# Performance work log

Hardware: AMD Instinct MI355X
Metric: run time of the kernel (lower is better)

Reference implementation:

```python
import jax, jax.numpy as jnp
import numpy as np

H, KD, VD, KNN = 8, 64, 64, 128
D, FC, N, S = 512, 2048, 4, 1024
GW_DEC, GW_ENC = 0.5, 0.5
EPS = 1e-5
SCALE = float(np.sqrt(KD))


def _layer_norm(x):
    # nn.LayerNorm(out_dim, eps=1e-5, elementwise_affine=False)
    m = jnp.mean(x, -1, keepdims=True)
    v = jnp.var(x, -1, keepdims=True)
    return (x - m) * jax.lax.rsqrt(v + EPS)


def _mha(x, Wk, bk, Wv, bv, Wo, bo, att_graph, gw, mask, Wq=None, bq=None, q_in=None):
    # x: [N,S,D]; per-head projections stacked: Wk [H,D,Kd], Wv [H,D,Vd]
    key = jnp.einsum('nsd,hdk->hnsk', x, Wk) + bk[:, None, None, :]
    value = jnp.einsum('nsd,hdv->hnsv', x, Wv) + bv[:, None, None, :]
    if q_in is None:
        query = key  # self-attention: query = key (as in the torch code)
    else:
        query = jnp.einsum('nqd,hdk->hnqk', q_in, Wq) + bq[:, None, None, :]
    # broadcast-mul-sum in torch == batched matmul
    att = jnp.einsum('hnqk,hnsk->hnqs', query, key) / SCALE  # [H,N,Q,S]
    if mask:
        qlen, slen = att.shape[-2], att.shape[-1]
        causal = jnp.arange(slen)[None, :] <= jnp.arange(qlen)[:, None]
        att = jnp.where(causal, att, -jnp.inf)
    # knn sparsification: keep top-KNN per row, rest -> -inf (equiv to topk+scatter for distinct values)
    thresh = jax.lax.top_k(att, KNN)[0][..., -1:]
    att = jnp.where(att >= thresh, att, -jnp.inf)
    att = jax.nn.softmax(att, axis=-1)
    # blend with precomputed (softmaxed) graph attention
    att = gw * att_graph + (1.0 - gw) * att
    ctx = jnp.einsum('hnqs,hnsv->hnqv', att, value)  # [H,N,Q,Vd]
    ctx = jnp.transpose(ctx, (1, 2, 0, 3)).reshape(ctx.shape[1], ctx.shape[2], H * VD)
    return ctx @ Wo + bo


def setup_inputs() -> dict:
    key = jax.random.key(0)
    ks = jax.random.split(key, 22)
    p = lambda k, shp: (0.02 * jax.random.normal(k, shp)).astype(jnp.float32)
    return {
        'z': jax.random.normal(ks[0], (N, S, D), jnp.float32),
        'y': jax.random.normal(ks[1], (N, S, D), jnp.float32),
        'graph_dec': jax.random.normal(ks[2], (S, S), jnp.float32),
        'graph_enc': jax.random.normal(ks[3], (S, S), jnp.float32),
        'dec_Wk': p(ks[4], (H, D, KD)), 'dec_bk': p(ks[5], (H, KD)),
        'dec_Wv': p(ks[6], (H, D, VD)), 'dec_bv': p(ks[7], (H, VD)),
        'dec_Wo': p(ks[8], (H * VD, D)), 'dec_bo': p(ks[9], (D,)),
        'enc_Wk': p(ks[10], (H, D, KD)), 'enc_bk': p(ks[11], (H, KD)),
        'enc_Wq': p(ks[12], (H, D, KD)), 'enc_bq': p(ks[13], (H, KD)),
        'enc_Wv': p(ks[14], (H, D, VD)), 'enc_bv': p(ks[15], (H, VD)),
        'enc_Wo': p(ks[16], (H * VD, D)), 'enc_bo': p(ks[17], (D,)),
        'fc_W1': p(ks[18], (D, FC)), 'fc_b1': p(ks[19], (FC,)),
        'fc_W2': p(ks[20], (FC, D)), 'fc_b2': p(ks[21], (D,)),
    }


def reference(z, y, graph_dec, graph_enc, dec_Wk, dec_bk, dec_Wv, dec_bv, dec_Wo, dec_bo, enc_Wk, enc_bk, enc_Wq, enc_bq, enc_Wv, enc_bv, enc_Wo, enc_bo, fc_W1, fc_b1, fc_W2, fc_b2):
    # graphs are row-softmaxed at construction time in the torch module
    gdec = jax.nn.softmax(graph_dec, axis=-1)
    genc = jax.nn.softmax(graph_enc, axis=-1)
    # 1) masked decoder self-attention on y
    h = _mha(y, dec_Wk, dec_bk, dec_Wv, dec_bv, dec_Wo, dec_bo, gdec, GW_DEC, True)
    h = _layer_norm(h + y)
    # 2) encoder-decoder attention: keys/values from z, query from h via query_keys (query_key=True)
    h2 = _mha(z, enc_Wk, enc_bk, enc_Wv, enc_bv, enc_Wo, enc_bo, genc, GW_ENC, False, enc_Wq, enc_bq, h)
    h2 = _layer_norm(h2 + h)
    # 3) two-layer MLP
    h3 = jax.nn.relu(h2 @ fc_W1 + fc_b1) @ fc_W2 + fc_b2
    return _layer_norm(h3 + h2)
```

## Files before the change

kernel.cpp:

```cpp
#include <hip/hip_runtime.h>
#include <stdint.h>

typedef short short8 __attribute__((ext_vector_type(8)));
typedef short short4v __attribute__((ext_vector_type(4)));
typedef float floatx4 __attribute__((ext_vector_type(4)));

#define H_  8
#define NB_ 4
#define S_  1024
#define D_  512
#define KD_ 64

__device__ __forceinline__ short f2bf(float f){
    unsigned u = __builtin_bit_cast(unsigned, f);
    u += 0x7fffu + ((u>>16)&1u);
    return (short)(u>>16);
}
__device__ __forceinline__ float wred_addf(float x){
    #pragma unroll
    for(int o=32;o>0;o>>=1) x += __shfl_xor(x,o,64);
    return x;
}
__device__ __forceinline__ float wred_maxf(float x){
    #pragma unroll
    for(int o=32;o>0;o>>=1) x = fmaxf(x,__shfl_xor(x,o,64));
    return x;
}
__device__ __forceinline__ unsigned bkey(unsigned u){
    return (u & 0x8000u) ? ((~u) & 0xffffu) : (u | 0x8000u);
}
__device__ __forceinline__ float key2f(unsigned k){
    unsigned u = (k & 0x8000u) ? (k & 0x7fffu) : ((~k) & 0xffffu);
    return __builtin_bit_cast(float, u<<16);
}

__global__ __launch_bounds__(256) void cvt2_kernel(const float* __restrict__ a, const float* __restrict__ b,
                                                   short* __restrict__ oa, short* __restrict__ ob){
    const float* in = blockIdx.y ? b : a;
    short* out = blockIdx.y ? ob : oa;
    int i = (blockIdx.x*256 + threadIdx.x)*4;
    floatx4 v = *(const floatx4*)(in + i);
    short4v r;
    #pragma unroll
    for(int j=0;j<4;j++) r[j] = f2bf(v[j]);
    *(short4v*)(out + i) = r;
}

__global__ __launch_bounds__(256) void wtrans5_kernel(
    const float* __restrict__ dWk, const float* __restrict__ dWv,
    const float* __restrict__ eWk, const float* __restrict__ eWv, const float* __restrict__ eWq,
    short* __restrict__ wKVd, short* __restrict__ wKVe, short* __restrict__ wQet)
{
    __shared__ float t[32][33];
    int zz = blockIdx.z; int w = zz>>3, h = zz&7;
    const float* src; short* dst;
    if(w==0){ src = dWk + h*32768; dst = wKVd + h*65536; }
    else if(w==1){ src = dWv + h*32768; dst = wKVd + h*65536 + 32768; }
    else if(w==2){ src = eWk + h*32768; dst = wKVe + h*65536; }
    else if(w==3){ src = eWv + h*32768; dst = wKVe + h*65536 + 32768; }
    else { src = eWq + h*32768; dst = wQet + h*32768; }
    const int R = 512, C = 64;
    int c0 = blockIdx.x*32, r0 = blockIdx.y*32;
    int tid = threadIdx.x;
    int r = tid>>3, cq = (tid&7)*4;
    #pragma unroll
    for(int i=0;i<4;i++) t[r][cq+i] = src[(r0+r)*C + c0+cq+i];
    __syncthreads();
    int c = tid>>3, rq = (tid&7)*4;
    #pragma unroll
    for(int i=0;i<4;i++) dst[(c0+c)*R + r0+rq+i] = f2bf(t[rq+i][c]);
}

__global__ __launch_bounds__(256) void wtrans4_kernel(
    const float* __restrict__ dWo, const float* __restrict__ eWo,
    const float* __restrict__ W1, const float* __restrict__ W2,
    short* __restrict__ oWod, short* __restrict__ oWoe,
    short* __restrict__ oW1, short* __restrict__ oW2)
{
    __shared__ float t[32][33];
    int id = blockIdx.x;
    const float* src; short* dst; int R, C, c0, r0;
    if(id < 512){
        src = (id<256)? dWo : eWo; dst = (id<256)? oWod : oWoe;
        int tt = id & 255; R = 512; C = 512;
        c0 = (tt&15)*32; r0 = (tt>>4)*32;
    } else if(id < 1536){
        src = W1; dst = oW1; int tt = id - 512; R = 512; C = 2048;
        c0 = (tt&63)*32; r0 = (tt>>6)*32;
    } else {
        src = W2; dst = oW2; int tt = id - 1536; R = 2048; C = 512;
        c0 = (tt&15)*32; r0 = (tt>>4)*32;
    }
    int tid = threadIdx.x;
    int r = tid>>3, cq = (tid&7)*4;
    #pragma unroll
    for(int i=0;i<4;i++) t[r][cq+i] = src[(long)(r0+r)*C + c0+cq+i];
    __syncthreads();
    int c = tid>>3, rq = (tid&7)*4;
    #pragma unroll
    for(int i=0;i<4;i++) dst[(long)(c0+c)*R + r0+rq+i] = f2bf(t[rq+i][c]);
}

__global__ __launch_bounds__(256) void graph_softmax_kernel(const float* __restrict__ g0,
                                                            const float* __restrict__ g1,
                                                            short* __restrict__ o0,
                                                            short* __restrict__ o1){
    int row = blockIdx.x;
    const float* g = blockIdx.y ? g1 : g0;
    short* o = blockIdx.y ? o1 : o0;
    const float* gr = g + (long)row*S_;
    short* orow = o + (long)row*S_;
    int tid = threadIdx.x, wave = tid>>6, lane = tid&63;
    __shared__ float red[8];
    float v[4]; float mx = -3.0e38f;
    #pragma unroll
    for(int i=0;i<4;i++){ v[i] = gr[tid + 256*i]; mx = fmaxf(mx, v[i]); }
    mx = wred_maxf(mx);
    if(lane==0) red[wave] = mx;
    __syncthreads();
    mx = fmaxf(fmaxf(red[0],red[1]), fmaxf(red[2],red[3]));
    float s = 0.f;
    #pragma unroll
    for(int i=0;i<4;i++){ v[i] = __expf(v[i]-mx); s += v[i]; }
    s = wred_addf(s);
    if(lane==0) red[4+wave] = s;
    __syncthreads();
    s = red[4]+red[5]+red[6]+red[7];
    float inv = 1.f/s;
    #pragma unroll
    for(int i=0;i<4;i++) orow[tid + 256*i] = f2bf(v[i]*inv);
}

template<int KV>
__global__ __launch_bounds__(256) void gemm_proj_kernel(
    const short* __restrict__ A, const short* __restrict__ Bt,
    const float* __restrict__ b1, const float* __restrict__ b2,
    short* __restrict__ o1, short* __restrict__ o2)
{
    constexpr int TN = KV ? 128 : 64;
    constexpr int NI = TN/32;
    __shared__ short As[64*32];
    __shared__ short Bs[TN*32];
    int z = blockIdx.z;
    int m0 = blockIdx.x*64;
    const short* Bb = Bt + (long)z*(TN*512);
    int tid = threadIdx.x, wave = tid>>6, lane = tid&63, quad = lane>>4, nl = lane&15;
    int wm = (wave&1)*32, wn = (wave>>1)*(TN/2);
    floatx4 acc[2][NI];
    #pragma unroll
    for(int i=0;i<2;i++)
        #pragma unroll
        for(int j=0;j<NI;j++) acc[i][j] = (floatx4){0.f,0.f,0.f,0.f};
    int r = tid>>2, c = (tid&3)*8;
    for(int k0=0;k0<512;k0+=32){
        __syncthreads();
        __builtin_amdgcn_global_load_lds(
            (const __attribute__((address_space(1))) unsigned*)(A + (long)(m0 + r)*512 + k0 + c),
            (__attribute__((address_space(3))) unsigned*)((char*)As + wave*1024), 16, 0, 0);
        #pragma unroll
        for(int i=0;i<TN/64;i++)
            __builtin_amdgcn_global_load_lds(
                (const __attribute__((address_space(1))) unsigned*)(Bb + (long)(r + i*64)*512 + k0 + c),
                (__attribute__((address_space(3))) unsigned*)((char*)Bs + i*4096 + wave*1024), 16, 0, 0);
        __syncthreads();
        short8 af[2], bfr[NI];
        #pragma unroll
        for(int i=0;i<2;i++) af[i] = *(const short8*)(As + (wm + i*16 + nl)*32 + quad*8);
        #pragma unroll
        for(int j=0;j<NI;j++) bfr[j] = *(const short8*)(Bs + (wn + j*16 + nl)*32 + quad*8);
        #pragma unroll
        for(int i=0;i<2;i++)
            #pragma unroll
            for(int j=0;j<NI;j++)
                acc[i][j] = __builtin_amdgcn_mfma_f32_16x16x32_bf16(af[i],bfr[j],acc[i][j],0,0,0);
    }
    #pragma unroll
    for(int j=0;j<NI;j++){
        int n = wn + j*16 + nl;
        float bv = (KV && n >= 64) ? b2[z*64 + n - 64] : b1[z*64 + n];
        #pragma unroll
        for(int i=0;i<2;i++){
            #pragma unroll
            for(int rr=0;rr<4;rr++){
                int m = m0 + wm + i*16 + quad*4 + rr;
                float v = acc[i][j][rr] + bv;
                long zb = (long)(z*NB_ + (m>>10));
                if(KV && n >= 64) o2[ (zb*KD_ + (n-64))*S_ + (m&1023) ] = f2bf(v);
                else              o1[ (zb*S_ + (m&1023))*KD_ + n ] = f2bf(v);
            }
        }
    }
}

template<int TM, int TN, int OUTBF, int RELU>
__global__ __launch_bounds__(256) void gemm_big_kernel(
    const short* __restrict__ A, const short* __restrict__ Bt, const float* __restrict__ bias,
    void* __restrict__ out, int M, int N, int K)
{
    __shared__ short As[TM*32];
    __shared__ short Bs[TN*32];
    int m0 = blockIdx.x*TM, n0 = blockIdx.y*TN;
    int tid = threadIdx.x, wave = tid>>6, lane = tid&63, quad = lane>>4, nl = lane&15;
    constexpr int MI = TM/32, NI = TN/32;
    int wm = (wave&1)*(TM/2), wn = (wave>>1)*(TN/2);
    floatx4 acc[MI][NI];
    #pragma unroll
    for(int i=0;i<MI;i++)
        #pragma unroll
        for(int j=0;j<NI;j++) acc[i][j] = (floatx4){0.f,0.f,0.f,0.f};

    int r = tid>>2, c = (tid&3)*8;
    for(int k0=0;k0<K;k0+=32){
        __syncthreads();
        #pragma unroll
        for(int i=0;i<TM/64;i++)
            __builtin_amdgcn_global_load_lds(
                (const __attribute__((address_space(1))) unsigned*)(A + (long)(m0 + r + i*64)*K + k0 + c),
                (__attribute__((address_space(3))) unsigned*)((char*)As + i*4096 + wave*1024),
                16, 0, 0);
        #pragma unroll
        for(int i=0;i<TN/64;i++)
            __builtin_amdgcn_global_load_lds(
                (const __attribute__((address_space(1))) unsigned*)(Bt + (long)(n0 + r + i*64)*K + k0 + c),
                (__attribute__((address_space(3))) unsigned*)((char*)Bs + i*4096 + wave*1024),
                16, 0, 0);
        __syncthreads();
        short8 af[MI], bfr[NI];
        #pragma unroll
        for(int i=0;i<MI;i++) af[i] = *(const short8*)(As + (wm + i*16 + nl)*32 + quad*8);
        #pragma unroll
        for(int j=0;j<NI;j++) bfr[j] = *(const short8*)(Bs + (wn + j*16 + nl)*32 + quad*8);
        #pragma unroll
        for(int i=0;i<MI;i++)
            #pragma unroll
            for(int j=0;j<NI;j++)
                acc[i][j] = __builtin_amdgcn_mfma_f32_16x16x32_bf16(af[i],bfr[j],acc[i][j],0,0,0);
    }
    #pragma unroll
    for(int j=0;j<NI;j++){
        int n = n0 + wn + j*16 + nl;
        float bv = bias[n];
        #pragma unroll
        for(int i=0;i<MI;i++){
            #pragma unroll
            for(int rr=0;rr<4;rr++){
                int m = m0 + wm + i*16 + quad*4 + rr;
                float v = acc[i][j][rr] + bv;
                if(RELU) v = fmaxf(v, 0.f);
                if(OUTBF) ((short*)out)[(long)m*N + n] = f2bf(v);
                else      ((float*)out)[(long)m*N + n] = v;
            }
        }
    }
}

__global__ __launch_bounds__(512,6) void attn_kernel(
    const short* __restrict__ Qb, const short* __restrict__ Kb, const short* __restrict__ Vt,
    const short* __restrict__ graph, short* __restrict__ ctx, int causal)
{
    __shared__ short attb[16*1024];
    __shared__ float pbuf[16*68];
    int hn = blockIdx.x, qt = blockIdx.y;
    int h = hn>>2, n = hn&3;
    int q0 = qt*16;
    int tid=threadIdx.x, wave=tid>>6, lane=tid&63, quad=lane>>4, nl=lane&15;

    const short* Qp = Qb + ((long)hn*S_ + q0 + nl)*KD_ + quad*8;
    short8 aq0 = *(const short8*)(Qp);
    short8 aq1 = *(const short8*)(Qp + 32);
    const short* Kp = Kb + (long)hn*S_*KD_;
    int stmax = causal ? qt : 63;
    for(int st=wave; st<=stmax; st+=8){
        const short* kp = Kp + (st*16 + nl)*KD_ + quad*8;
        short8 b0 = *(const short8*)(kp);
        short8 b1 = *(const short8*)(kp + 32);
        floatx4 cc = (floatx4){0.f,0.f,0.f,0.f};
        cc = __builtin_amdgcn_mfma_f32_16x16x32_bf16(aq0,b0,cc,0,0,0);
        cc = __builtin_amdgcn_mfma_f32_16x16x32_bf16(aq1,b1,cc,0,0,0);
        #pragma unroll
        for(int rr=0;rr<4;rr++){
            int q = quad*4 + rr, s = st*16 + nl;
            attb[q*1024 + ((s + 8*q)&1023)] = f2bf(cc[rr]*0.125f);
        }
    }
    __syncthreads();

    for(int rp=0; rp<2; ++rp){
        int q = wave*2 + rp;
        int qg = q0 + q;
        int slimit = causal ? qg : 1023;
        short* rowp = attb + q*1024;
        int sb = lane*16;
        int p0 = (sb + 8*q) & 1023;
        short8 c0 = *(const short8*)(rowp + p0);
        short8 c1 = *(const short8*)(rowp + ((p0+8)&1023));
        unsigned mv[16];
        unsigned mk = 0u;
        #pragma unroll
        for(int j=0;j<8;j++){
            unsigned k0 = (sb+j   <= slimit) ? bkey((unsigned)(unsigned short)c0[j]) : 0u;
            unsigned k1 = (sb+8+j <= slimit) ? bkey((unsigned)(unsigned short)c1[j]) : 0u;
            mv[j]   = k0; mk = k0>mk?k0:mk;
            mv[8+j] = k1; mk = k1>mk?k1:mk;
        }
        #pragma unroll
        for(int o=32;o>0;o>>=1){ unsigned tt=__shfl_xor(mk,o,64); mk = tt>mk?tt:mk; }
        unsigned lo=0u, hi=mk+1u;
        for(int it=0; it<16; ++it){
            unsigned mid = lo + ((hi-lo)>>1);
            unsigned cnt = 0u;
            #pragma unroll
            for(int j=0;j<16;j++) cnt += (mv[j] >= mid) ? 1u : 0u;
            #pragma unroll
            for(int o=32;o>0;o>>=1) cnt += __shfl_xor(cnt,o,64);
            bool ge = (cnt >= 128u);
            bool eq = (cnt == 128u);
            lo = ge ? mid : lo;
            hi = ge ? (eq ? mid+1u : hi) : mid;
        }
        float mxf = key2f(mk);
        float sm = 0.f;
        #pragma unroll
        for(int j=0;j<16;j++){
            unsigned k = mv[j];
            float e = (k >= lo && k != 0u) ? __expf(key2f(k)-mxf) : 0.f;
            mv[j] = __builtin_bit_cast(unsigned, e);
            sm += e;
        }
        #pragma unroll
        for(int o=32;o>0;o>>=1) sm += __shfl_xor(sm,o,64);
        float inv = 0.5f/sm;
        const short* grow = graph + (long)qg*1024 + sb;
        short8 g0 = *(const short8*)(grow);
        short8 g1 = *(const short8*)(grow + 8);
        short8 o0, o1;
        #pragma unroll
        for(int j=0;j<8;j++){
            float gv0 = __builtin_bit_cast(float, ((unsigned)(unsigned short)g0[j])<<16);
            float gv1 = __builtin_bit_cast(float, ((unsigned)(unsigned short)g1[j])<<16);
            float e0 = __builtin_bit_cast(float, mv[j]);
            float e1 = __builtin_bit_cast(float, mv[8+j]);
            o0[j] = f2bf(0.5f*gv0 + e0*inv);
            o1[j] = f2bf(0.5f*gv1 + e1*inv);
        }
        *(short8*)(rowp + p0) = o0;
        *(short8*)(rowp + ((p0+8)&1023)) = o1;
    }
    __syncthreads();

    int vh = wave & 3, sh = wave >> 2;
    int v0 = vh*16;
    const short* Vp = Vt + ((long)hn*KD_ + v0 + nl)*S_;
    floatx4 o4 = (floatx4){0.f,0.f,0.f,0.f};
    int arow = nl;
    int sbase = sh*512;
    for(int s0=sbase; s0<sbase+512; s0+=32){
        int cs = (s0 + quad*8 + 8*arow) & 1023;
        short8 ap = *(const short8*)(attb + arow*1024 + cs);
        short8 bv = *(const short8*)(Vp + s0 + quad*8);
        o4 = __builtin_amdgcn_mfma_f32_16x16x32_bf16(ap,bv,o4,0,0,0);
    }
    if(sh==1){
        #pragma unroll
        for(int rr=0;rr<4;rr++) pbuf[(quad*4+rr)*68 + v0 + nl] = o4[rr];
    }
    __syncthreads();
    if(sh==0){
        #pragma unroll
        for(int rr=0;rr<4;rr++){
            int q = quad*4 + rr;
            float v = o4[rr] + pbuf[q*68 + v0 + nl];
            ctx[ ((long)(n*S_ + q0 + q))*512 + h*KD_ + v0 + nl ] = f2bf(v);
        }
    }
}

__global__ __launch_bounds__(256) void ln_kernel(const float* __restrict__ x, const float* __restrict__ res,
                                                 float* __restrict__ outf, short* __restrict__ outb){
    long row = blockIdx.x;
    const float* xr = x + row*D_;
    const float* rr = res + row*D_;
    int tid = threadIdx.x, wave = tid>>6, lane = tid&63;
    float t0 = xr[tid] + rr[tid];
    float t1 = xr[tid+256] + rr[tid+256];
    float s = t0 + t1, s2 = t0*t0 + t1*t1;
    __shared__ float red[8];
    s = wred_addf(s); s2 = wred_addf(s2);
    if(lane==0){ red[wave] = s; red[4+wave] = s2; }
    __syncthreads();
    s  = red[0]+red[1]+red[2]+red[3];
    s2 = red[4]+red[5]+red[6]+red[7];
    float mean = s*(1.f/512.f);
    float var = s2*(1.f/512.f) - mean*mean;
    float rs = rsqrtf(var + 1e-5f);
    float o0 = (t0-mean)*rs, o1 = (t1-mean)*rs;
    if(outf){ outf[row*D_+tid] = o0; outf[row*D_+tid+256] = o1; }
    if(outb){ outb[row*D_+tid] = f2bf(o0); outb[row*D_+tid+256] = f2bf(o1); }
}

extern "C" void kernel_launch(void* const* d_in, const int* in_sizes, int n_in,
                              void* d_out, int out_size, void* d_ws, size_t ws_size,
                              hipStream_t stream)
{
    const float* z         = (const float*)d_in[0];
    const float* y         = (const float*)d_in[1];
    const float* graph_dec = (const float*)d_in[2];
    const float* graph_enc = (const float*)d_in[3];
    const float* dec_Wk = (const float*)d_in[4];  const float* dec_bk = (const float*)d_in[5];
    const float* dec_Wv = (const float*)d_in[6];  const float* dec_bv = (const float*)d_in[7];
    const float* dec_Wo = (const float*)d_in[8];  const float* dec_bo = (const float*)d_in[9];
    const float* enc_Wk = (const float*)d_in[10]; const float* enc_bk = (const float*)d_in[11];
    const float* enc_Wq = (const float*)d_in[12]; const float* enc_bq = (const float*)d_in[13];
    const float* enc_Wv = (const float*)d_in[14]; const float* enc_bv = (const float*)d_in[15];
    const float* enc_Wo = (const float*)d_in[16]; const float* enc_bo = (const float*)d_in[17];
    const float* fc_W1  = (const float*)d_in[18]; const float* fc_b1  = (const float*)d_in[19];
    const float* fc_W2  = (const float*)d_in[20]; const float* fc_b2  = (const float*)d_in[21];

    char* ws = (char*)d_ws;
    short* gdec  = (short*)(ws + 0x0000000);
    short* genc  = (short*)(ws + 0x0400000);
    short* y_bf  = (short*)(ws + 0x0800000);
    short* z_bf  = (short*)(ws + 0x0C00000);
    short* Kdec  = (short*)(ws + 0x1000000);
    short* Vtdec = (short*)(ws + 0x1400000);
    short* Kenc  = (short*)(ws + 0x1800000);
    short* Vtenc = (short*)(ws + 0x1C00000);
    short* Qenc  = (short*)(ws + 0x2000000);
    short* ctx   = (short*)(ws + 0x2400000);
    float* tmp   = (float*)(ws + 0x2800000);
    float* hbuf  = (float*)(ws + 0x3000000);
    short* h_bf  = (short*)(ws + 0x3800000);
    float* h2    = (float*)(ws + 0x3C00000);
    short* h2_bf = (short*)(ws + 0x4400000);
    short* fc1   = (short*)(ws + 0x4800000);
    short* wKVd  = (short*)(ws + 0x5800000);
    short* wKVe  = (short*)(ws + 0x5900000);
    short* wQet  = (short*)(ws + 0x5A00000);
    short* wOdt  = (short*)(ws + 0x5A80000);
    short* wOet  = (short*)(ws + 0x5B00000);
    short* wF1t  = (short*)(ws + 0x5B80000);
    short* wF2t  = (short*)(ws + 0x5D80000);
    float* outp  = (float*)d_out;

    dim3 B(256);
    wtrans5_kernel<<<dim3(2,16,40),B,0,stream>>>(dec_Wk, dec_Wv, enc_Wk, enc_Wv, enc_Wq, wKVd, wKVe, wQet);
    wtrans4_kernel<<<dim3(2560),B,0,stream>>>(dec_Wo, enc_Wo, fc_W1, fc_W2, wOdt, wOet, wF1t, wF2t);
    cvt2_kernel<<<dim3(2048,2),B,0,stream>>>(y, z, y_bf, z_bf);
    graph_softmax_kernel<<<dim3(1024,2),B,0,stream>>>(graph_dec, graph_enc, gdec, genc);
    gemm_proj_kernel<1><<<dim3(64,1,8),B,0,stream>>>(y_bf, wKVd, dec_bk, dec_bv, Kdec, Vtdec);
    attn_kernel<<<dim3(32,64),dim3(512),0,stream>>>(Kdec, Kdec, Vtdec, gdec, ctx, 1);
    gemm_big_kernel<64,128,0,0><<<dim3(64,4),B,0,stream>>>(ctx, wOdt, dec_bo, tmp, 4096, 512, 512);
    ln_kernel<<<dim3(4096),B,0,stream>>>(tmp, y, hbuf, h_bf);
    gemm_proj_kernel<1><<<dim3(64,1,8),B,0,stream>>>(z_bf, wKVe, enc_bk, enc_bv, Kenc, Vtenc);
    gemm_proj_kernel<0><<<dim3(64,1,8),B,0,stream>>>(h_bf, wQet, enc_bq, (const float*)0, Qenc, (short*)0);
    attn_kernel<<<dim3(32,64),dim3(512),0,stream>>>(Qenc, Kenc, Vtenc, genc, ctx, 0);
    gemm_big_kernel<64,128,0,0><<<dim3(64,4),B,0,stream>>>(ctx, wOet, enc_bo, tmp, 4096, 512, 512);
    ln_kernel<<<dim3(4096),B,0,stream>>>(tmp, hbuf, h2, h2_bf);
    gemm_big_kernel<128,128,1,1><<<dim3(32,16),B,0,stream>>>(h2_bf, wF1t, fc_b1, fc1, 4096, 2048, 512);
    gemm_big_kernel<64,128,0,0><<<dim3(64,4),B,0,stream>>>(fc1, wF2t, fc_b2, tmp, 4096, 512, 2048);
    ln_kernel<<<dim3(4096),B,0,stream>>>(tmp, h2, outp, (short*)0);
}
```

Before: 429.4 us.

## Speed up attention top-k selection with DPP reductions and packed bf16 math

Rewrites the per-row top-k threshold and softmax blend in the attention kernel. It uses DPP-based wave reductions instead of shuffles, packed bit tricks for the bf16 key transform, and a binary search that exits early once the range narrows. Causal masking is now applied by pre-filling and writing -inf in the score buffer, so the per-element masking branch in the selection loop goes away. The 0.5 graph weight is folded into the graph softmax, and packed bf16 conversion is used on output. There are risks: the pre-fill adds an extra barrier and LDS store pass for causal blocks, and the search loop now has a data-dependent trip count.

```diff
diff --git a/kernel.cpp b/kernel.cpp
--- a/kernel.cpp
+++ b/kernel.cpp
@@ -4,6 +4,7 @@
 typedef short short8 __attribute__((ext_vector_type(8)));
 typedef short short4v __attribute__((ext_vector_type(4)));
 typedef float floatx4 __attribute__((ext_vector_type(4)));
+typedef unsigned uint4v __attribute__((ext_vector_type(4)));
 
 #define H_  8
 #define NB_ 4
@@ -26,12 +27,46 @@
     for(int o=32;o>0;o>>=1) x = fmaxf(x,__shfl_xor(x,o,64));
     return x;
 }
-__device__ __forceinline__ unsigned bkey(unsigned u){
-    return (u & 0x8000u) ? ((~u) & 0xffffu) : (u | 0x8000u);
-}
-__device__ __forceinline__ float key2f(unsigned k){
-    unsigned u = (k & 0x8000u) ? (k & 0x7fffu) : ((~k) & 0xffffu);
-    return __builtin_bit_cast(float, u<<16);
+__device__ __forceinline__ unsigned umaxu(unsigned a, unsigned b){ return a>b?a:b; }
+
+template<int CTRL, int RMASK, int BC>
+__device__ __forceinline__ unsigned dppu(unsigned x){
+    return (unsigned)__builtin_amdgcn_update_dpp(0, (int)x, CTRL, RMASK, 0xf, BC);
+}
+__device__ __forceinline__ unsigned wsum_dpp_u(unsigned x){
+    x += dppu<0x111,0xf,1>(x);
+    x += dppu<0x112,0xf,1>(x);
+    x += dppu<0x114,0xf,1>(x);
+    x += dppu<0x118,0xf,1>(x);
+    x += dppu<0x142,0xa,0>(x);
+    x += dppu<0x143,0xc,0>(x);
+    return (unsigned)__builtin_amdgcn_readlane((int)x, 63);
+}
+__device__ __forceinline__ unsigned wmax_dpp_u(unsigned x){
+    x = umaxu(x, dppu<0x111,0xf,1>(x));
+    x = umaxu(x, dppu<0x112,0xf,1>(x));
+    x = umaxu(x, dppu<0x114,0xf,1>(x));
+    x = umaxu(x, dppu<0x118,0xf,1>(x));
+    x = umaxu(x, dppu<0x142,0xa,0>(x));
+    x = umaxu(x, dppu<0x143,0xc,0>(x));
+    return (unsigned)__builtin_amdgcn_readlane((int)x, 63);
+}
+__device__ __forceinline__ float addu_f(float a, unsigned b){
+    return a + __builtin_bit_cast(float, b);
+}
+__device__ __forceinline__ float wsum_dpp_f(float x){
+    x = addu_f(x, dppu<0x111,0xf,1>(__builtin_bit_cast(unsigned,x)));
+    x = addu_f(x, dppu<0x112,0xf,1>(__builtin_bit_cast(unsigned,x)));
+    x = addu_f(x, dppu<0x114,0xf,1>(__builtin_bit_cast(unsigned,x)));
+    x = addu_f(x, dppu<0x118,0xf,1>(__builtin_bit_cast(unsigned,x)));
+    x = addu_f(x, dppu<0x142,0xa,0>(__builtin_bit_cast(unsigned,x)));
+    x = addu_f(x, dppu<0x143,0xc,0>(__builtin_bit_cast(unsigned,x)));
+    return __builtin_bit_cast(float, (unsigned)__builtin_amdgcn_readlane((int)__builtin_bit_cast(unsigned, x), 63));
+}
+__device__ __forceinline__ unsigned cvt_pk_bf16(float a, float b){
+    unsigned r;
+    asm("v_cvt_pk_bf16_f32 %0, %1, %2" : "=v"(r) : "v"(a), "v"(b));
+    return r;
 }
 
 __global__ __launch_bounds__(256) void cvt2_kernel(const float* __restrict__ a, const float* __restrict__ b,
@@ -126,7 +161,7 @@
     if(lane==0) red[4+wave] = s;
     __syncthreads();
     s = red[4]+red[5]+red[6]+red[7];
-    float inv = 1.f/s;
+    float inv = 0.5f/s;
     #pragma unroll
     for(int i=0;i<4;i++) orow[tid + 256*i] = f2bf(v[i]*inv);
 }
@@ -265,6 +300,13 @@
     int q0 = qt*16;
     int tid=threadIdx.x, wave=tid>>6, lane=tid&63, quad=lane>>4, nl=lane&15;
 
+    if(causal){
+        uint4v fv = (uint4v){0xff80ff80u,0xff80ff80u,0xff80ff80u,0xff80ff80u};
+        #pragma unroll
+        for(int i=0;i<4;i++) *(uint4v*)((char*)attb + tid*16 + i*8192) = fv;
+        __syncthreads();
+    }
+
     const short* Qp = Qb + ((long)hn*S_ + q0 + nl)*KD_ + quad*8;
     short8 aq0 = *(const short8*)(Qp);
     short8 aq1 = *(const short8*)(Qp + 32);
@@ -277,74 +319,86 @@
         floatx4 cc = (floatx4){0.f,0.f,0.f,0.f};
         cc = __builtin_amdgcn_mfma_f32_16x16x32_bf16(aq0,b0,cc,0,0,0);
         cc = __builtin_amdgcn_mfma_f32_16x16x32_bf16(aq1,b1,cc,0,0,0);
+        int s = st*16 + nl;
         #pragma unroll
         for(int rr=0;rr<4;rr++){
-            int q = quad*4 + rr, s = st*16 + nl;
-            attb[q*1024 + ((s + 8*q)&1023)] = f2bf(cc[rr]*0.125f);
-        }
-    }
-    __syncthreads();
-
+            int q = quad*4 + rr;
+            short val = f2bf(cc[rr]*0.125f);
+            if(causal && s > q0 + q) val = (short)0xff80;
+            attb[q*1024 + ((s + 8*q)&1023)] = val;
+        }
+    }
+    __syncthreads();
+
+    #pragma unroll 1
     for(int rp=0; rp<2; ++rp){
         int q = wave*2 + rp;
         int qg = q0 + q;
-        int slimit = causal ? qg : 1023;
         short* rowp = attb + q*1024;
         int sb = lane*16;
         int p0 = (sb + 8*q) & 1023;
-        short8 c0 = *(const short8*)(rowp + p0);
-        short8 c1 = *(const short8*)(rowp + ((p0+8)&1023));
-        unsigned mv[16];
-        unsigned mk = 0u;
-        #pragma unroll
-        for(int j=0;j<8;j++){
-            unsigned k0 = (sb+j   <= slimit) ? bkey((unsigned)(unsigned short)c0[j]) : 0u;
-            unsigned k1 = (sb+8+j <= slimit) ? bkey((unsigned)(unsigned short)c1[j]) : 0u;
-            mv[j]   = k0; mk = k0>mk?k0:mk;
-            mv[8+j] = k1; mk = k1>mk?k1:mk;
-        }
-        #pragma unroll
-        for(int o=32;o>0;o>>=1){ unsigned tt=__shfl_xor(mk,o,64); mk = tt>mk?tt:mk; }
-        unsigned lo=0u, hi=mk+1u;
-        for(int it=0; it<16; ++it){
-            unsigned mid = lo + ((hi-lo)>>1);
-            unsigned cnt = 0u;
+        uint4v u0 = *(const uint4v*)(rowp + p0);
+        uint4v u1 = *(const uint4v*)(rowp + ((p0+8)&1023));
+        unsigned pr[8];
+        #pragma unroll
+        for(int i=0;i<4;i++){ pr[i] = u0[i]; pr[4+i] = u1[i]; }
+        unsigned kv[16];
+        #pragma unroll
+        for(int i=0;i<8;i++){
+            unsigned u = pr[i];
+            unsigned kp = u ^ (0x80008000u + ((u>>15)&0x00010001u)*0x7fffu);
+            kv[2*i]   = kp & 0xffffu;
+            kv[2*i+1] = kp >> 16;
+        }
+        unsigned a0 = umaxu(kv[0],kv[1]),  a1 = umaxu(kv[2],kv[3]);
+        unsigned a2 = umaxu(kv[4],kv[5]),  a3 = umaxu(kv[6],kv[7]);
+        unsigned a4 = umaxu(kv[8],kv[9]),  a5 = umaxu(kv[10],kv[11]);
+        unsigned a6 = umaxu(kv[12],kv[13]),a7 = umaxu(kv[14],kv[15]);
+        unsigned mk = umaxu(umaxu(umaxu(a0,a1),umaxu(a2,a3)), umaxu(umaxu(a4,a5),umaxu(a6,a7)));
+        unsigned mks = wmax_dpp_u(mk);
+        unsigned lo = 0u, hi = mks + 1u;
+        while(hi - lo > 1u){
+            unsigned mid = (lo + hi) >> 1;
+            unsigned c = 0u;
             #pragma unroll
-            for(int j=0;j<16;j++) cnt += (mv[j] >= mid) ? 1u : 0u;
-            #pragma unroll
-            for(int o=32;o>0;o>>=1) cnt += __shfl_xor(cnt,o,64);
-            bool ge = (cnt >= 128u);
-            bool eq = (cnt == 128u);
-            lo = ge ? mid : lo;
-            hi = ge ? (eq ? mid+1u : hi) : mid;
-        }
-        float mxf = key2f(mk);
-        float sm = 0.f;
-        #pragma unroll
-        for(int j=0;j<16;j++){
-            unsigned k = mv[j];
-            float e = (k >= lo && k != 0u) ? __expf(key2f(k)-mxf) : 0.f;
-            mv[j] = __builtin_bit_cast(unsigned, e);
-            sm += e;
-        }
-        #pragma unroll
-        for(int o=32;o>0;o>>=1) sm += __shfl_xor(sm,o,64);
-        float inv = 0.5f/sm;
+            for(int j=0;j<16;j++) c += (unsigned)(kv[j] >= mid);
+            unsigned tot = wsum_dpp_u(c);
+            if(tot >= 128u) lo = mid; else hi = mid;
+        }
+        unsigned uo = (mks & 0x8000u) ? ((mks & 0x7fffu)<<16) : ((~mks)<<16);
+        float mxf = __builtin_bit_cast(float, uo);
+        float ev[16]; float sm = 0.f;
+        #pragma unroll
+        for(int i=0;i<8;i++){
+            float f0 = __builtin_bit_cast(float, pr[i] << 16);
+            float f1 = __builtin_bit_cast(float, pr[i] & 0xffff0000u);
+            float e0 = __expf(f0 - mxf);
+            float e1 = __expf(f1 - mxf);
+            e0 = (kv[2*i]   >= lo) ? e0 : 0.f;
+            e1 = (kv[2*i+1] >= lo) ? e1 : 0.f;
+            ev[2*i] = e0; ev[2*i+1] = e1;
+            sm += e0 + e1;
+        }
+        sm = wsum_dpp_f(sm);
+        float inv = 0.5f / sm;
         const short* grow = graph + (long)qg*1024 + sb;
-        short8 g0 = *(const short8*)(grow);
-        short8 g1 = *(const short8*)(grow + 8);
-        short8 o0, o1;
-        #pragma unroll
-        for(int j=0;j<8;j++){
-            float gv0 = __builtin_bit_cast(float, ((unsigned)(unsigned short)g0[j])<<16);
-            float gv1 = __builtin_bit_cast(float, ((unsigned)(unsigned short)g1[j])<<16);
-            float e0 = __builtin_bit_cast(float, mv[j]);
-            float e1 = __builtin_bit_cast(float, mv[8+j]);
-            o0[j] = f2bf(0.5f*gv0 + e0*inv);
-            o1[j] = f2bf(0.5f*gv1 + e1*inv);
-        }
-        *(short8*)(rowp + p0) = o0;
-        *(short8*)(rowp + ((p0+8)&1023)) = o1;
+        uint4v g0 = *(const uint4v*)(grow);
+        uint4v g1 = *(const uint4v*)(grow + 8);
+        unsigned gp[8];
+        #pragma unroll
+        for(int i=0;i<4;i++){ gp[i] = g0[i]; gp[4+i] = g1[i]; }
+        uint4v w0, w1;
+        #pragma unroll
+        for(int i=0;i<8;i++){
+            float gl = __builtin_bit_cast(float, gp[i] << 16);
+            float gh = __builtin_bit_cast(float, gp[i] & 0xffff0000u);
+            float r0 = fmaf(ev[2*i],   inv, gl);
+            float r1 = fmaf(ev[2*i+1], inv, gh);
+            unsigned pk = cvt_pk_bf16(r0, r1);
+            if(i<4) w0[i] = pk; else w1[i-4] = pk;
+        }
+        *(uint4v*)(rowp + p0) = w0;
+        *(uint4v*)(rowp + ((p0+8)&1023)) = w1;
     }
     __syncthreads();
 
```

Result: faster. 394.4 us (-8.1%).
